# Kernel tuning notes

Hardware: AMD Instinct MI355X
Metric: run time of the kernel (lower is better)

Reference implementation:

```python
import jax, jax.numpy as jnp
import numpy as np
from jax.scipy.linalg import solve_triangular

B, L, HID, NH = 2, 1024, 1024, 4
DK = DV = 256
CONV_K, CHUNK, FIR_S_K, FIR_L_K = 4, 32, 3, 31
GATE_IN = HID + 3 * DV * 4 + DV * 4  # 5120
GATE_H = 2 * DV  # 512


def _l2norm(x):
    return x * jax.lax.rsqrt(jnp.sum(x * x, -1, keepdims=True) + 1e-6)


def _short_conv(x, w):
    # causal depthwise conv1d + silu. x: [b,l,c], w: [c,k]
    c, k = w.shape
    y = jax.lax.conv_general_dilated(x.transpose(0, 2, 1), w[:, None, :], (1,),
                                     [(k - 1, 0)], feature_group_count=c)
    return jax.nn.silu(y.transpose(0, 2, 1))


def _fir(x, f):
    # per-head depthwise causal FIR. x: [b,l,h,d], f: [h,d,k]
    b, l, h, d = x.shape
    k = f.shape[-1]
    xf = x.transpose(0, 2, 3, 1).reshape(b, h * d, l)
    y = jax.lax.conv_general_dilated(xf, f.reshape(h * d, 1, k), (1,),
                                     [(k - 1, 0)], feature_group_count=h * d)
    return y.reshape(b, h, d, l).transpose(0, 3, 1, 2)


def _delta_rule(q, k, v, beta, chunk=CHUNK):
    # q,k: [b,h,L,dk], v: [b,h,L,dv], beta: [b,h,L]; L % chunk == 0
    b, h, l, dk = q.shape
    dv = v.shape[-1]
    n = l // chunk
    q = _l2norm(q)
    k = _l2norm(k)
    v = v * beta[..., None]
    kb = k * beta[..., None]
    rs = lambda t: t.reshape(b, h, n, chunk, -1)
    q, k, v, kb = map(rs, (q, k, v, kb))
    # UT transform: serial forward substitution == unit-lower triangular solve
    A = -jnp.tril(jnp.einsum('bhncd,bhned->bhnce', kb, k), -1)  # strictly lower
    eye = jnp.eye(chunk, dtype=q.dtype)
    T = solve_triangular(eye - A, jnp.broadcast_to(eye, A.shape), lower=True)
    u = T @ v   # [b,h,n,c,dv]
    w = T @ kb  # [b,h,n,c,dk]
    mov = lambda t: jnp.moveaxis(t, 2, 0)

    def step(S, inp):
        qi, ki, ui, wi = inp  # [b,h,c,d]
        attn = jnp.tril(qi @ ki.transpose(0, 1, 3, 2))  # causal incl. diag
        u_i = ui - wi @ S
        o_i = qi @ S + attn @ u_i
        return S + ki.transpose(0, 1, 3, 2) @ u_i, o_i

    S0 = jnp.zeros((b, h, dk, dv), dtype=q.dtype)
    S, o = jax.lax.scan(step, S0, (mov(q), mov(k), mov(u), mov(w)))
    o = jnp.moveaxis(o, 0, 2).reshape(b, h, l, dv)
    return o, S


def _gate(hidden, branches, W1, b1, W2, b2, temp, eps_floor):
    def stats(p):
        m = p.mean(-1, keepdims=True)
        r = jnp.sqrt(jnp.clip((p * p).mean(-1, keepdims=True), 1e-8))
        mx = p.max(-1, keepdims=True)
        return jnp.concatenate([jnp.broadcast_to(m, p.shape),
                                jnp.broadcast_to(r, p.shape),
                                jnp.broadcast_to(mx, p.shape)], -1)

    b, l, h, d = branches[0].shape
    hb = jnp.broadcast_to(hidden[:, :, None, :], (b, l, h, hidden.shape[-1]))
    head_in = jnp.concatenate([hb] + [stats(p) for p in branches] + list(branches), -1)
    hmid = jax.nn.gelu(head_in @ W1 + b1, approximate=False)
    logits = hmid @ W2 + b2  # [b,l,h,4]
    t = jnp.clip(temp, 0.2, 10.0)[None, None, :, None]
    w = jax.nn.softmax(logits / t, -1)
    floor = jnp.clip(eps_floor, 1e-7, 0.1)[None, None]
    w = jnp.maximum(w, floor)
    return w / w.sum(-1, keepdims=True)


def setup_inputs() -> dict:
    key = jax.random.key(0)
    ks = jax.random.split(key, 16)
    s = 0.02
    inp = {
        'x': jax.random.normal(ks[0], (B, L, HID), jnp.float32),
        'Wq': jax.random.normal(ks[1], (HID, NH * DK), jnp.float32) * s,
        'Wk': jax.random.normal(ks[2], (HID, NH * DK), jnp.float32) * s,
        'Wv': jax.random.normal(ks[3], (HID, NH * DV), jnp.float32) * s,
        'Wb': jax.random.normal(ks[4], (HID, NH), jnp.float32) * s,
        'qc_w': jax.random.normal(ks[5], (NH * DK, CONV_K), jnp.float32) * 0.5,
        'kc_w': jax.random.normal(ks[6], (NH * DK, CONV_K), jnp.float32) * 0.5,
        'vc_w': jax.random.normal(ks[7], (NH * DV, CONV_K), jnp.float32) * 0.5,
        'gW1': jax.random.normal(ks[10], (GATE_IN, GATE_H), jnp.float32) * s,
        'gb1': jnp.zeros((GATE_H,), jnp.float32),
        'gW2': jax.random.normal(ks[11], (GATE_H, 4), jnp.float32) * s,
        'gb2': jnp.zeros((4,), jnp.float32),
        'temp': jnp.ones((NH,), jnp.float32),
        'eps_floor': jnp.full((NH, 4), 0.01, jnp.float32),
        'onorm_w': jnp.ones((DV,), jnp.float32),
        'Wo': jax.random.normal(ks[12], (NH * DV, HID), jnp.float32) * s,
    }
    # FIR filters: identity tap at last position + small noise (matches init intent)
    fs = jnp.zeros((NH, DV, FIR_S_K)).at[..., -1].set(1.0)
    fl = jnp.zeros((NH, DV, FIR_L_K)).at[..., -1].set(1.0)
    inp['fir_s'] = fs + s * jax.random.normal(ks[8], fs.shape, jnp.float32)
    inp['fir_l'] = fl + s * jax.random.normal(ks[9], fl.shape, jnp.float32)
    return inp


def reference(x, Wq, Wk, Wv, Wb, qc_w, kc_w, vc_w, fir_s, fir_l,
              gW1, gb1, gW2, gb2, temp, eps_floor, onorm_w, Wo):
    b, l, _ = x.shape
    q = _short_conv(x @ Wq, qc_w).reshape(b, l, NH, DK)
    k = _short_conv(x @ Wk, kc_w).reshape(b, l, NH, DK)
    v = _short_conv(x @ Wv, vc_w).reshape(b, l, NH, DV)
    beta = jax.nn.sigmoid(x @ Wb)  # [b,l,h]
    tr = lambda t: t.transpose(0, 2, 1, 3)
    delta_o, _ = _delta_rule(tr(q), tr(k), tr(v), beta.transpose(0, 2, 1))
    delta_o = tr(delta_o)  # [b,l,h,dv]
    branches = [_fir(v, fir_s), _fir(v, fir_l), delta_o, v]
    w = _gate(x, branches, gW1, gb1, gW2, gb2, temp, eps_floor)
    o = sum(w[..., i:i + 1] * branches[i] for i in range(4))
    o = o * jax.lax.rsqrt((o * o).mean(-1, keepdims=True) + 1e-5) * onorm_w
    return o.reshape(b, l, NH * DV) @ Wo
```

## Files before the change

kernel.cpp:

```cpp
#include <hip/hip_runtime.h>
#include <math.h>

#define BB 2
#define LL 1024
#define HIDD 1024
#define NH 4
#define DD 256
#define NCH 32
#define ROWS 2048
#define HROWS 8192

typedef long long i64;
typedef unsigned short u16t;
typedef unsigned int u32t;
typedef __attribute__((ext_vector_type(8))) short short8;
typedef __attribute__((ext_vector_type(4))) float f32x4;
#define MFMA_BF16(a, b, c) __builtin_amdgcn_mfma_f32_16x16x32_bf16(a, b, c, 0, 0, 0)

__device__ __forceinline__ float sigmoidf_(float x) { return 1.0f / (1.0f + expf(-x)); }

__device__ __forceinline__ u16t f2bf(float f) {
  u32t u = __float_as_uint(f);
  u = u + 0x7FFFu + ((u >> 16) & 1u);
  return (u16t)(u >> 16);
}
__device__ __forceinline__ u32t pk2(u16t a, u16t b) { return (u32t)a | ((u32t)b << 16); }

__device__ __forceinline__ u32t cvt_pk_bf16(float lo, float hi) {
  u32t r;
  asm("v_cvt_pk_bf16_f32 %0, %1, %2" : "=v"(r) : "v"(lo), "v"(hi));
  return r;
}

__device__ __forceinline__ void barrier_lds_only() {
  asm volatile("s_waitcnt lgkmcnt(0)" ::: "memory");
  __builtin_amdgcn_s_barrier();
  asm volatile("" ::: "memory");
}

template<int N>
__device__ __forceinline__ void block_reduce_sum(float* v, float* scratch) {
  int lane = threadIdx.x & 63, wid = threadIdx.x >> 6;
#pragma unroll
  for (int i = 0; i < N; i++) {
    float x = v[i];
#pragma unroll
    for (int off = 1; off < 64; off <<= 1) x += __shfl_xor(x, off);
    if (lane == 0) scratch[wid * N + i] = x;
  }
  __syncthreads();
#pragma unroll
  for (int i = 0; i < N; i++)
    v[i] = scratch[i] + scratch[N + i] + scratch[2 * N + i] + scratch[3 * N + i];
  __syncthreads();
}

__device__ __forceinline__ void transcast_body(
    const float* __restrict__ in, int ldin, u16t* __restrict__ out, int ldout,
    int nbi, int kbi, float (*tile)[33]) {
  int tx = threadIdx.x & 31, ty = threadIdx.x >> 5;
  int nb = nbi * 32, kb = kbi * 32;
#pragma unroll
  for (int r = 0; r < 4; r++)
    tile[ty + r * 8][tx] = in[(i64)(kb + ty + r * 8) * ldin + nb + tx];
  __syncthreads();
#pragma unroll
  for (int r = 0; r < 4; r++)
    out[(i64)(nb + ty + r * 8) * ldout + kb + tx] = f2bf(tile[tx][ty + r * 8]);
}

__global__ __launch_bounds__(256) void prep_kernel(
    const float* __restrict__ Wq, const float* __restrict__ Wk, const float* __restrict__ Wv,
    const float* __restrict__ x,
    u16t* __restrict__ WqkvT, u16t* __restrict__ xbf) {
  __shared__ float tile[32][33];
  int blk = blockIdx.x, t = threadIdx.x;
  if (blk < 3072) {
    int m = blk >> 10, bi = blk & 1023;
    const float* in = m == 0 ? Wq : m == 1 ? Wk : Wv;
    transcast_body(in, 1024, WqkvT + (i64)m * 1024 * 1024, 1024, bi & 31, bi >> 5, tile);
  } else {
    i64 e = ((i64)(blk - 3072) * 256 + t) * 4;
    float4 v = *(const float4*)(x + e);
    uint2 o;
    o.x = pk2(f2bf(v.x), f2bf(v.y));
    o.y = pk2(f2bf(v.z), f2bf(v.w));
    *(uint2*)(xbf + e) = o;
  }
}

__device__ __forceinline__ void gemm_bt_body(
    const u16t* __restrict__ A, const u16t* __restrict__ B,
    float* __restrict__ C, int K, int ldc, int n0, int m0,
    u16t* As, u16t* Bs) {
  int t = threadIdx.x;
  int w = t >> 6, lane = t & 63;
  int l15 = lane & 15, quad = lane >> 4;
  int wm = (w & 1) * 64, wn = (w >> 1) * 64;
  f32x4 acc[4][4] = {};
  int srow = t >> 1, shalf = (t & 1) * 16;
  const u16t* Ag = A + (i64)(m0 + srow) * K + shalf;
  const u16t* Bg = B + (i64)(n0 + srow) * K + shalf;
  for (int k0 = 0; k0 < K; k0 += 32) {
    *(uint4*)&As[srow * 40 + shalf] = *(const uint4*)(Ag + k0);
    *(uint4*)&As[srow * 40 + shalf + 8] = *(const uint4*)(Ag + k0 + 8);
    *(uint4*)&Bs[srow * 40 + shalf] = *(const uint4*)(Bg + k0);
    *(uint4*)&Bs[srow * 40 + shalf + 8] = *(const uint4*)(Bg + k0 + 8);
    __syncthreads();
    short8 a[4], b[4];
#pragma unroll
    for (int mt = 0; mt < 4; mt++)
      a[mt] = *(const short8*)&As[(wm + mt * 16 + l15) * 40 + quad * 8];
#pragma unroll
    for (int nt = 0; nt < 4; nt++)
      b[nt] = *(const short8*)&Bs[(wn + nt * 16 + l15) * 40 + quad * 8];
#pragma unroll
    for (int mt = 0; mt < 4; mt++)
#pragma unroll
      for (int nt = 0; nt < 4; nt++)
        acc[mt][nt] = MFMA_BF16(a[mt], b[nt], acc[mt][nt]);
    __syncthreads();
  }
#pragma unroll
  for (int mt = 0; mt < 4; mt++) {
    int r0 = m0 + wm + mt * 16 + quad * 4;
#pragma unroll
    for (int nt = 0; nt < 4; nt++) {
      int cc = n0 + wn + nt * 16 + l15;
#pragma unroll
      for (int rg = 0; rg < 4; rg++)
        C[(i64)(r0 + rg) * ldc + cc] = acc[mt][nt][rg];
    }
  }
}

__global__ __launch_bounds__(256) void gemm_bt_kernel(
    const u16t* __restrict__ A, const u16t* __restrict__ B,
    float* __restrict__ C, int K, int ldc) {
  __shared__ u16t As[128 * 40];
  __shared__ u16t Bs[128 * 40];
  gemm_bt_body(A, B, C, K, ldc, blockIdx.x * 128, blockIdx.y * 128, As, Bs);
}

__global__ __launch_bounds__(256) void conv_silu3_kernel(
    const float* __restrict__ pre, const float* __restrict__ qw,
    const float* __restrict__ kw, const float* __restrict__ vw,
    float* __restrict__ qo, float* __restrict__ ko, float* __restrict__ vo,
    u16t* __restrict__ brcat) {
  int seg = blockIdx.x >> 11;
  int row = blockIdx.x & 2047;
  int l = row & 1023;
  int c = threadIdx.x * 4;
  const float* w = seg == 0 ? qw : seg == 1 ? kw : vw;
  float* out = seg == 0 ? qo : seg == 1 ? ko : vo;
  float4 w0 = *(const float4*)(w + (i64)(c + 0) * 4);
  float4 w1 = *(const float4*)(w + (i64)(c + 1) * 4);
  float4 w2 = *(const float4*)(w + (i64)(c + 2) * 4);
  float4 w3 = *(const float4*)(w + (i64)(c + 3) * 4);
  const float* base = pre + (i64)row * 3072 + (seg << 10) + c;
  float4 x0 = *(const float4*)(base);
  float4 acc;
  acc.x = w0.w * x0.x; acc.y = w1.w * x0.y; acc.z = w2.w * x0.z; acc.w = w3.w * x0.w;
  if (l >= 1) {
    float4 xm = *(const float4*)(base - 3072);
    acc.x += w0.z * xm.x; acc.y += w1.z * xm.y; acc.z += w2.z * xm.z; acc.w += w3.z * xm.w;
  }
  if (l >= 2) {
    float4 xm = *(const float4*)(base - 2 * 3072);
    acc.x += w0.y * xm.x; acc.y += w1.y * xm.y; acc.z += w2.y * xm.z; acc.w += w3.y * xm.w;
  }
  if (l >= 3) {
    float4 xm = *(const float4*)(base - 3 * 3072);
    acc.x += w0.x * xm.x; acc.y += w1.x * xm.y; acc.z += w2.x * xm.z; acc.w += w3.x * xm.w;
  }
  float4 r;
  r.x = acc.x * sigmoidf_(acc.x);
  r.y = acc.y * sigmoidf_(acc.y);
  r.z = acc.z * sigmoidf_(acc.z);
  r.w = acc.w * sigmoidf_(acc.w);
  *(float4*)(out + (i64)row * 1024 + c) = r;
  if (seg == 2) {
    uint2 o;
    o.x = cvt_pk_bf16(r.x, r.y);
    o.y = cvt_pk_bf16(r.z, r.w);
    *(uint2*)(brcat + ((i64)row * 4 + (c >> 8)) * 1024 + 768 + (c & 255)) = o;
  }
}

__global__ __launch_bounds__(256) void beta_kernel(
    const float* __restrict__ x, const float* __restrict__ Wb, float* __restrict__ beta) {
  int row = blockIdx.x, t = threadIdx.x;
  __shared__ float sc[16];
  float a[4] = {0, 0, 0, 0};
  for (int c = t; c < 1024; c += 256) {
    float xv = x[(i64)row * 1024 + c];
    float4 wv = *(const float4*)(Wb + c * 4);
    a[0] += xv * wv.x; a[1] += xv * wv.y; a[2] += xv * wv.z; a[3] += xv * wv.w;
  }
  block_reduce_sum<4>(a, sc);
  if (t == 0) {
#pragma unroll
    for (int g = 0; g < 4; g++) beta[row * 4 + g] = sigmoidf_(a[g]);
  }
}

__global__ __launch_bounds__(256) void preprocess_kernel(
    const float* __restrict__ q, const float* __restrict__ k, const float* __restrict__ v,
    const float* __restrict__ beta, float* __restrict__ qn, float* __restrict__ kn,
    float* __restrict__ vb, float* __restrict__ kb, u16t* __restrict__ qnbf) {
  int t = threadIdx.x, lane = t & 63, wv = t >> 6;
  int row = blockIdx.x * 4 + wv;
  i64 base = (i64)row * 256 + lane * 4;
  float4 q4 = *(const float4*)(q + base);
  float4 k4 = *(const float4*)(k + base);
  float4 v4 = *(const float4*)(v + base);
  float s2[2];
  s2[0] = q4.x * q4.x + q4.y * q4.y + q4.z * q4.z + q4.w * q4.w;
  s2[1] = k4.x * k4.x + k4.y * k4.y + k4.z * k4.z + k4.w * k4.w;
#pragma unroll
  for (int off = 1; off < 64; off <<= 1) {
    s2[0] += __shfl_xor(s2[0], off);
    s2[1] += __shfl_xor(s2[1], off);
  }
  float qi = rsqrtf(s2[0] + 1e-6f), ki = rsqrtf(s2[1] + 1e-6f);
  float bet = beta[row];
  float4 qn4, kn4, vb4, kb4;
  qn4.x = q4.x * qi; qn4.y = q4.y * qi; qn4.z = q4.z * qi; qn4.w = q4.w * qi;
  kn4.x = k4.x * ki; kn4.y = k4.y * ki; kn4.z = k4.z * ki; kn4.w = k4.w * ki;
  vb4.x = v4.x * bet; vb4.y = v4.y * bet; vb4.z = v4.z * bet; vb4.w = v4.w * bet;
  kb4.x = kn4.x * bet; kb4.y = kn4.y * bet; kb4.z = kn4.z * bet; kb4.w = kn4.w * bet;
  *(float4*)(qn + base) = qn4;
  *(float4*)(kn + base) = kn4;
  *(float4*)(vb + base) = vb4;
  *(float4*)(kb + base) = kb4;
  int b = row >> 12, l = (row >> 2) & 1023, h = row & 3;
  uint2 o;
  o.x = cvt_pk_bf16(qn4.x, qn4.y);
  o.y = cvt_pk_bf16(qn4.z, qn4.w);
  *(uint2*)(qnbf + ((i64)(b * 4 + h) * 1024 + l) * 256 + lane * 4) = o;
}

__global__ __launch_bounds__(256) void phaseA_kernel(
    const float* __restrict__ qn, const float* __restrict__ kn,
    const float* __restrict__ vb, const float* __restrict__ kb,
    float* __restrict__ u_g, u16t* __restrict__ w_bf, u16t* __restrict__ attn_bf,
    u16t* __restrict__ knT) {
  __shared__ float KN[32][260];
  __shared__ float Ms[32][32];
  int blk = blockIdx.x, t = threadIdx.x;
  int i = blk & 31, bh = blk >> 5;
  int rbase = ((bh >> 2) * LL + i * 32) * NH + (bh & 3);
  i64 bhn = blk;
#pragma unroll
  for (int ii = 0; ii < 8; ii++) {
    int fid = t + ii * 256;
    int c = fid >> 6, dq = (fid & 63) << 2;
    *(float4*)&KN[c][dq] = *(const float4*)(kn + (i64)(rbase + c * NH) * 256 + dq);
  }
  __syncthreads();
  int c = t >> 3, e0 = (t & 7) * 4;
  const float* kbp = kb + (i64)(rbase + c * NH) * 256;
  const float* qp = qn + (i64)(rbase + c * NH) * 256;
  float am[4] = {0, 0, 0, 0}, aa[4] = {0, 0, 0, 0};
  for (int d = 0; d < 256; d += 4) {
    float4 kv = *(const float4*)(kbp + d);
    float4 qv = *(const float4*)(qp + d);
#pragma unroll
    for (int z = 0; z < 4; z++) {
      float4 nv = *(const float4*)&KN[e0 + z][d];
      am[z] += kv.x * nv.x + kv.y * nv.y + kv.z * nv.z + kv.w * nv.w;
      aa[z] += qv.x * nv.x + qv.y * nv.y + qv.z * nv.z + qv.w * nv.w;
    }
  }
  {
    uint2 o;
    u16t a0 = (e0 + 0 <= c) ? f2bf(aa[0]) : 0;
    u16t a1 = (e0 + 1 <= c) ? f2bf(aa[1]) : 0;
    u16t a2 = (e0 + 2 <= c) ? f2bf(aa[2]) : 0;
    u16t a3 = (e0 + 3 <= c) ? f2bf(aa[3]) : 0;
    o.x = pk2(a0, a1); o.y = pk2(a2, a3);
    *(uint2*)(attn_bf + bhn * 1024 + c * 32 + e0) = o;
  }
#pragma unroll
  for (int z = 0; z < 4; z++) {
    int e = e0 + z;
    Ms[c][e] = (e < c) ? am[z] : 0.0f;
  }
  __syncthreads();
  float uc[32], wc[32];
#pragma unroll
  for (int cc = 0; cc < 32; cc++) {
    float uval = vb[(i64)(rbase + cc * NH) * 256 + t];
    float wval = kb[(i64)(rbase + cc * NH) * 256 + t];
#pragma unroll
    for (int c2 = 0; c2 < cc; c2++) {
      float m = Ms[cc][c2];
      uval -= m * uc[c2];
      wval -= m * wc[c2];
    }
    uc[cc] = uval; wc[cc] = wval;
    u_g[(bhn * 32 + cc) * 256 + t] = uval;
    w_bf[(bhn * 32 + cc) * 256 + t] = f2bf(-wval);
  }
  int d = t;
  u16t o[32];
#pragma unroll
  for (int cc = 0; cc < 32; cc++) o[cc] = f2bf(KN[cc][d]);
#pragma unroll
  for (int z = 0; z < 4; z++) {
    uint4 vv;
    vv.x = pk2(o[z * 8 + 0], o[z * 8 + 1]);
    vv.y = pk2(o[z * 8 + 2], o[z * 8 + 3]);
    vv.z = pk2(o[z * 8 + 4], o[z * 8 + 5]);
    vv.w = pk2(o[z * 8 + 6], o[z * 8 + 7]);
    *(uint4*)(knT + (bhn * 256 + d) * 32 + z * 8) = vv;
  }
}

#define SROW 264
struct ScanBuf {
  short8 m8[8];
  f32x4 uc4;
  short8 af;
  short8 kf[4];
};

__device__ void delta_scan_body(
    int blk,
    const u16t* __restrict__ wbf, const u16t* __restrict__ knT,
    const float* __restrict__ u_g, const u16t* __restrict__ qnbf,
    const u16t* __restrict__ attnbf,
    float* __restrict__ dlt, u16t* __restrict__ brcat,
    u16t* Sbf, u16t* Ubf) {
  int t = threadIdx.x, w = t >> 6, lane = t & 63;
  int l15 = lane & 15, quad = lane >> 4;
  int bh = blk & 7, jb = blk >> 3, j0 = jb * 16;
  int b_ = bh >> 2, h_ = bh & 3;
  bool isU = (w < 2);
  int wc = isU ? w : (w - 2);
  for (int idx = t; idx < 16 * SROW; idx += 256) Sbf[idx] = 0;
  f32x4 accS[4] = {};
  __syncthreads();
  __builtin_amdgcn_s_setprio(1);

  auto load_chunk = [&](int i, ScanBuf& B) {
    i64 bhn = (i64)bh * 32 + i;
    const u16t* mbase = isU
        ? wbf + (bhn * 32 + wc * 16 + l15) * 256 + quad * 8
        : qnbf + ((i64)bh * 1024 + i * 32 + wc * 16 + l15) * 256 + quad * 8;
#pragma unroll
    for (int kd = 0; kd < 8; kd++) B.m8[kd] = *(const short8*)(mbase + kd * 32);
    if (isU) {
      int cm = wc * 16 + quad * 4;
#pragma unroll
      for (int r = 0; r < 4; r++)
        B.uc4[r] = u_g[(bhn * 32 + cm + r) * 256 + j0 + l15];
    } else {
      B.af = *(const short8*)(attnbf + bhn * 1024 + (wc * 16 + l15) * 32 + quad * 8);
    }
#pragma unroll
    for (int dt = 0; dt < 4; dt++)
      B.kf[dt] = *(const short8*)(knT + (bhn * 256 + w * 64 + dt * 16 + l15) * 32 + quad * 8);
  };

  auto process = [&](int i, ScanBuf& B) {
    f32x4 zero = {};
    f32x4 ca = isU ? B.uc4 : zero;
    f32x4 cb = zero;
#pragma unroll
    for (int kd = 0; kd < 4; kd++) {
      short8 sfa = *(const short8*)&Sbf[l15 * SROW + kd * 32 + quad * 8];
      short8 sfb = *(const short8*)&Sbf[l15 * SROW + (kd + 4) * 32 + quad * 8];
      ca = MFMA_BF16(B.m8[kd], sfa, ca);
      cb = MFMA_BF16(B.m8[kd + 4], sfb, cb);
    }
    f32x4 cacc;
#pragma unroll
    for (int r = 0; r < 4; r++) cacc[r] = ca[r] + cb[r];
    if (isU) {
      int cm = wc * 16 + quad * 4;
      uint2 o;
      o.x = cvt_pk_bf16(cacc[0], cacc[1]);
      o.y = cvt_pk_bf16(cacc[2], cacc[3]);
      *(uint2*)&Ubf[l15 * 40 + cm] = o;
    }
    barrier_lds_only();
    short8 bu = *(const short8*)&Ubf[l15 * 40 + quad * 8];
    if (!isU) {
      cacc = MFMA_BF16(B.af, bu, cacc);
#pragma unroll
      for (int rg = 0; rg < 4; rg++) {
        int l = i * 32 + wc * 16 + quad * 4 + rg;
        i64 row = ((i64)b_ * 1024 + l) * 4 + h_;
        dlt[row * 256 + j0 + l15] = cacc[rg];
        brcat[row * 1024 + 512 + j0 + l15] = f2bf(cacc[rg]);
      }
    }
#pragma unroll
    for (int dt = 0; dt < 4; dt++) accS[dt] = MFMA_BF16(B.kf[dt], bu, accS[dt]);
#pragma unroll
    for (int dt = 0; dt < 4; dt++) {
      uint2 o;
      o.x = cvt_pk_bf16(accS[dt][0], accS[dt][1]);
      o.y = cvt_pk_bf16(accS[dt][2], accS[dt][3]);
      *(uint2*)&Sbf[l15 * SROW + w * 64 + dt * 16 + quad * 4] = o;
    }
    barrier_lds_only();
  };

  ScanBuf b0, b1;
  load_chunk(0, b0);
#pragma unroll 1
  for (int ii = 0; ii < 16; ii++) {
    int i = ii * 2;
    load_chunk(i + 1, b1);
    process(i, b0);
    if (ii < 15) load_chunk(i + 2, b0);
    process(i + 1, b1);
  }
  __builtin_amdgcn_s_setprio(0);
}

__device__ void fir2_body(
    int blk, const float* __restrict__ v,
    const float* __restrict__ f_s, const float* __restrict__ f_l,
    float* __restrict__ fs, float* __restrict__ fl, u16t* __restrict__ brcat) {
  int t = threadIdx.x;
  int b = blk >> 8, h = (blk >> 6) & 3, lc = blk & 63;
  int l0 = lc * 16;
  float flw[31], fsw[3];
  const float* flp = f_l + ((i64)h * 256 + t) * 31;
#pragma unroll
  for (int j = 0; j < 31; j++) flw[j] = flp[j];
  const float* fsp = f_s + ((i64)h * 256 + t) * 3;
#pragma unroll
  for (int j = 0; j < 3; j++) fsw[j] = fsp[j];
  float win[46];
#pragma unroll
  for (int r = 0; r < 46; r++) {
    int l = l0 - 30 + r;
    win[r] = (l >= 0) ? v[(((i64)b * 1024 + l) * 4 + h) * 256 + t] : 0.0f;
  }
#pragma unroll
  for (int i = 0; i < 16; i++) {
    float al = 0.0f;
#pragma unroll
    for (int j = 0; j < 31; j++) al += flw[j] * win[i + j];
    float as = fsw[0] * win[i + 28] + fsw[1] * win[i + 29] + fsw[2] * win[i + 30];
    i64 row = ((i64)b * 1024 + (l0 + i)) * 4 + h;
    fs[row * 256 + t] = as;
    fl[row * 256 + t] = al;
    brcat[row * 1024 + t] = f2bf(as);
    brcat[row * 1024 + 256 + t] = f2bf(al);
  }
}

__global__ __launch_bounds__(256) void mega2_kernel(
    const u16t* __restrict__ wbf, const u16t* __restrict__ knT,
    const float* __restrict__ u_g, const u16t* __restrict__ qnbf,
    const u16t* __restrict__ attnbf, float* __restrict__ dlt, u16t* __restrict__ brcat,
    const float* __restrict__ vbuf, const float* __restrict__ firs,
    const float* __restrict__ firl, float* __restrict__ fs, float* __restrict__ fl,
    const float* __restrict__ gW1, const float* __restrict__ Wo,
    u16t* __restrict__ W1hT, u16t* __restrict__ W1bT, u16t* __restrict__ WoT,
    float* __restrict__ wsum) {
  __shared__ __attribute__((aligned(16))) char smem[9728];
  int blk = blockIdx.x;
  if (blk < 128) {
    u16t* Sbf = (u16t*)smem;
    u16t* Ubf = Sbf + 16 * SROW;
    delta_scan_body(blk, wbf, knT, u_g, qnbf, attnbf, dlt, brcat, Sbf, Ubf);
  } else if (blk < 640) {
    fir2_body(blk - 128, vbuf, firs, firl, fs, fl, brcat);
  } else if (blk < 2688) {
    float (*tile)[33] = (float(*)[33])smem;
    int pb = blk - 640;
    if (pb < 1024) {
      int which = pb >> 9, bi = pb & 511;
      const float* in = gW1 + (which ? (i64)4096 * 512 : 0);
      transcast_body(in, 512, which ? W1bT : W1hT, 1024, bi & 15, bi >> 4, tile);
    } else {
      int bi = pb - 1024;
      transcast_body(Wo, 1024, WoT, 1024, bi & 31, bi >> 5, tile);
    }
  } else {
    int bi = blk - 2688;
    int s12 = bi >> 1, col = (bi & 1) * 256 + threadIdx.x;
    const float* p = gW1 + (i64)(1024 + s12 * 256) * 512 + col;
    float acc = 0.0f;
    for (int r = 0; r < 256; r++) acc += p[(i64)r * 512];
    wsum[s12 * 512 + col] = acc;
  }
}

__global__ __launch_bounds__(256) void gemm2_kernel(
    const u16t* __restrict__ xbf, const u16t* __restrict__ W1hT,
    float* __restrict__ hbase,
    const u16t* __restrict__ brcat, const u16t* __restrict__ W1bT,
    float* __restrict__ branchW) {
  __shared__ u16t As[128 * 40];
  __shared__ u16t Bs[128 * 40];
  int blk = blockIdx.x;
  if (blk < 64) {
    gemm_bt_body(xbf, W1hT, hbase, 1024, 512, (blk & 3) * 128, (blk >> 2) * 128, As, Bs);
  } else {
    int bi = blk - 64;
    gemm_bt_body(brcat, W1bT, branchW, 1024, 512, (bi & 3) * 128, (bi >> 2) * 128, As, Bs);
  }
}

__global__ __launch_bounds__(256) void gatemix_kernel(
    const float* __restrict__ hbase, const float* __restrict__ brW,
    const float* __restrict__ wsum,
    const float* __restrict__ gb1, const float* __restrict__ gW2,
    const float* __restrict__ gb2, const float* __restrict__ temp,
    const float* __restrict__ epsf,
    const float* __restrict__ fs, const float* __restrict__ fl,
    const float* __restrict__ dlt, const float* __restrict__ v,
    const float* __restrict__ onw, u16t* __restrict__ out) {
  int t = threadIdx.x, lane = t & 63, wv = t >> 6;
  int row = blockIdx.x * 4 + wv;
  int bl = row >> 2, h = row & 3;
  i64 base = (i64)row * 256 + lane * 4;
  float4 vfs = *(const float4*)(fs + base);
  float4 vfl = *(const float4*)(fl + base);
  float4 vdl = *(const float4*)(dlt + base);
  float4 vvv = *(const float4*)(v + base);
  float r8[8];
  r8[0] = vfs.x + vfs.y + vfs.z + vfs.w;
  r8[1] = vfs.x * vfs.x + vfs.y * vfs.y + vfs.z * vfs.z + vfs.w * vfs.w;
  r8[2] = vfl.x + vfl.y + vfl.z + vfl.w;
  r8[3] = vfl.x * vfl.x + vfl.y * vfl.y + vfl.z * vfl.z + vfl.w * vfl.w;
  r8[4] = vdl.x + vdl.y + vdl.z + vdl.w;
  r8[5] = vdl.x * vdl.x + vdl.y * vdl.y + vdl.z * vdl.z + vdl.w * vdl.w;
  r8[6] = vvv.x + vvv.y + vvv.z + vvv.w;
  r8[7] = vvv.x * vvv.x + vvv.y * vvv.y + vvv.z * vvv.z + vvv.w * vvv.w;
#pragma unroll
  for (int off = 1; off < 64; off <<= 1) {
#pragma unroll
    for (int i = 0; i < 8; i++) r8[i] += __shfl_xor(r8[i], off);
  }
  float m4[4];
  m4[0] = fmaxf(fmaxf(vfs.x, vfs.y), fmaxf(vfs.z, vfs.w));
  m4[1] = fmaxf(fmaxf(vfl.x, vfl.y), fmaxf(vfl.z, vfl.w));
  m4[2] = fmaxf(fmaxf(vdl.x, vdl.y), fmaxf(vdl.z, vdl.w));
  m4[3] = fmaxf(fmaxf(vvv.x, vvv.y), fmaxf(vvv.z, vvv.w));
#pragma unroll
  for (int off = 1; off < 64; off <<= 1) {
#pragma unroll
    for (int i = 0; i < 4; i++) m4[i] = fmaxf(m4[i], __shfl_xor(m4[i], off));
  }
  float st[12];
#pragma unroll
  for (int p = 0; p < 4; p++) {
    st[p * 3 + 0] = r8[p * 2] * (1.0f / 256.0f);
    st[p * 3 + 1] = sqrtf(fmaxf(r8[p * 2 + 1] * (1.0f / 256.0f), 1e-8f));
    st[p * 3 + 2] = m4[p];
  }
  float lg[4] = {0, 0, 0, 0};
#pragma unroll
  for (int jj = 0; jj < 8; jj++) {
    int o = jj * 64 + lane;
    float hm = hbase[(i64)bl * 512 + o] + brW[(i64)row * 512 + o] + gb1[o];
#pragma unroll
    for (int s = 0; s < 12; s++) hm += st[s] * wsum[s * 512 + o];
    float ge = 0.5f * hm * (1.0f + erff(hm * 0.70710678118654752f));
    float4 w2 = *(const float4*)(gW2 + o * 4);
    lg[0] += ge * w2.x; lg[1] += ge * w2.y; lg[2] += ge * w2.z; lg[3] += ge * w2.w;
  }
#pragma unroll
  for (int off = 1; off < 64; off <<= 1) {
#pragma unroll
    for (int i = 0; i < 4; i++) lg[i] += __shfl_xor(lg[i], off);
  }
  float tt = fminf(fmaxf(temp[h], 0.2f), 10.0f);
  float l0 = (lg[0] + gb2[0]) / tt;
  float l1 = (lg[1] + gb2[1]) / tt;
  float l2 = (lg[2] + gb2[2]) / tt;
  float l3 = (lg[3] + gb2[3]) / tt;
  float m = fmaxf(fmaxf(l0, l1), fmaxf(l2, l3));
  float e0 = expf(l0 - m), e1 = expf(l1 - m), e2 = expf(l2 - m), e3 = expf(l3 - m);
  float ssum = e0 + e1 + e2 + e3;
  float w0 = e0 / ssum, w1 = e1 / ssum, w2 = e2 / ssum, w3 = e3 / ssum;
  w0 = fmaxf(w0, fminf(fmaxf(epsf[h * 4 + 0], 1e-7f), 0.1f));
  w1 = fmaxf(w1, fminf(fmaxf(epsf[h * 4 + 1], 1e-7f), 0.1f));
  w2 = fmaxf(w2, fminf(fmaxf(epsf[h * 4 + 2], 1e-7f), 0.1f));
  w3 = fmaxf(w3, fminf(fmaxf(epsf[h * 4 + 3], 1e-7f), 0.1f));
  float s2 = w0 + w1 + w2 + w3;
  float g0 = w0 / s2, g1 = w1 / s2, g2 = w2 / s2, g3 = w3 / s2;
  float4 o4;
  o4.x = g0 * vfs.x + g1 * vfl.x + g2 * vdl.x + g3 * vvv.x;
  o4.y = g0 * vfs.y + g1 * vfl.y + g2 * vdl.y + g3 * vvv.y;
  o4.z = g0 * vfs.z + g1 * vfl.z + g2 * vdl.z + g3 * vvv.z;
  o4.w = g0 * vfs.w + g1 * vfl.w + g2 * vdl.w + g3 * vvv.w;
  float ss = o4.x * o4.x + o4.y * o4.y + o4.z * o4.z + o4.w * o4.w;
#pragma unroll
  for (int off = 1; off < 64; off <<= 1) ss += __shfl_xor(ss, off);
  float scale = rsqrtf(ss * (1.0f / 256.0f) + 1e-5f);
  float4 ow4 = *(const float4*)(onw + lane * 4);
  uint2 ow;
  ow.x = cvt_pk_bf16(o4.x * scale * ow4.x, o4.y * scale * ow4.y);
  ow.y = cvt_pk_bf16(o4.z * scale * ow4.z, o4.w * scale * ow4.w);
  *(uint2*)(out + (i64)bl * 1024 + h * 256 + lane * 4) = ow;
}

extern "C" void kernel_launch(void* const* d_in, const int* in_sizes, int n_in,
                              void* d_out, int out_size, void* d_ws, size_t ws_size,
                              hipStream_t stream) {
  (void)in_sizes; (void)n_in; (void)out_size; (void)ws_size;
  const float* x    = (const float*)d_in[0];
  const float* Wq   = (const float*)d_in[1];
  const float* Wk   = (const float*)d_in[2];
  const float* Wv   = (const float*)d_in[3];
  const float* Wb   = (const float*)d_in[4];
  const float* qcw  = (const float*)d_in[5];
  const float* kcw  = (const float*)d_in[6];
  const float* vcw  = (const float*)d_in[7];
  const float* gW1  = (const float*)d_in[8];
  const float* gb1  = (const float*)d_in[9];
  const float* gW2  = (const float*)d_in[10];
  const float* gb2  = (const float*)d_in[11];
  const float* temp = (const float*)d_in[12];
  const float* epsf = (const float*)d_in[13];
  const float* onw  = (const float*)d_in[14];
  const float* Wo   = (const float*)d_in[15];
  const float* firs = (const float*)d_in[16];
  const float* firl = (const float*)d_in[17];
  float* out = (float*)d_out;

  float* ws = (float*)d_ws;
  float* qkv_pre  = ws + 0;
  float* branchW  = ws + 0;
  float* hbase    = ws + 4194304;
  u16t*  brcat    = (u16t*)(ws + 6291456);
  float* qbuf     = ws + 10485760; float* qn = qbuf;
  float* kbuf     = ws + 12582912; float* kn = kbuf;
  float* vbuf     = ws + 14680064;
  float* vb       = ws + 16777216;
  u16t*  omix_bf  = (u16t*)(ws + 16777216);
  u16t*  W1hT     = (u16t*)(ws + 17825792);
  u16t*  W1bT     = (u16t*)(ws + 18087936);
  u16t*  WoT      = (u16t*)(ws + 18350080);
  float* kb       = ws + 18874368;
  float* dlt      = ws + 18874368;
  float* u_g      = ws + 20971520;
  u16t*  w_bf     = (u16t*)(ws + 23068672);
  u16t*  qn_bf    = (u16t*)(ws + 24117248);
  u16t*  knT      = (u16t*)(ws + 25165824);
  u16t*  attn_bf  = (u16t*)(ws + 26214400);
  float* fs       = ws + 26345472;
  float* fl       = ws + 28442624;
  u16t*  xbf      = (u16t*)(ws + 30539776);
  u16t*  WqkvT    = (u16t*)(ws + 31588352);
  float* betab    = ws + 33161216;
  float* wsum     = ws + 33267712;

  prep_kernel<<<5120, 256, 0, stream>>>(Wq, Wk, Wv, x, WqkvT, xbf);
  gemm_bt_kernel<<<dim3(24, 16), 256, 0, stream>>>(xbf, WqkvT, qkv_pre, 1024, 3072);
  conv_silu3_kernel<<<6144, 256, 0, stream>>>(qkv_pre, qcw, kcw, vcw, qbuf, kbuf, vbuf, brcat);
  beta_kernel<<<2048, 256, 0, stream>>>(x, Wb, betab);
  preprocess_kernel<<<2048, 256, 0, stream>>>(qbuf, kbuf, vbuf, betab, qn, kn, vb, kb, qn_bf);
  phaseA_kernel<<<256, 256, 0, stream>>>(qn, kn, vb, kb, u_g, w_bf, attn_bf, knT);
  mega2_kernel<<<2712, 256, 0, stream>>>(w_bf, knT, u_g, qn_bf, attn_bf, dlt, brcat,
                                         vbuf, firs, firl, fs, fl,
                                         gW1, Wo, W1hT, W1bT, WoT, wsum);
  gemm2_kernel<<<320, 256, 0, stream>>>(xbf, W1hT, hbase, brcat, W1bT, branchW);
  gatemix_kernel<<<2048, 256, 0, stream>>>(hbase, branchW, wsum, gb1, gW2, gb2,
                                           temp, epsf, fs, fl, dlt, vbuf, onw, omix_bf);
  gemm_bt_kernel<<<dim3(8, 16), 256, 0, stream>>>(omix_bf, WoT, out, 1024, 1024);
}
```

Measured before the change: 342.1 us.

## Rebalance kernel fusion: fold beta into prep, overlap weight transposes and hidden GEMM

Merges the beta projection into the prep kernel, moves the gate/output weight transpose-casts and wsum reduction into the phaseA kernel (which only had 256 working blocks), and moves the hidden-state gate GEMM into the scan/FIR mega kernel. The branch GEMM becomes a standalone launch. The intent is to fill idle CUs during the low-parallelism phaseA and delta scan and to cut one launch, at the cost of larger shared memory in the merged kernels and workspace buffers relocated.

Result: no change. 342.8 us (+0.2%).

```diff
diff --git a/kernel.cpp b/kernel.cpp
--- a/kernel.cpp
+++ b/kernel.cpp
@@ -71,21 +71,34 @@
 
 __global__ __launch_bounds__(256) void prep_kernel(
     const float* __restrict__ Wq, const float* __restrict__ Wk, const float* __restrict__ Wv,
-    const float* __restrict__ x,
-    u16t* __restrict__ WqkvT, u16t* __restrict__ xbf) {
+    const float* __restrict__ x, const float* __restrict__ Wb,
+    u16t* __restrict__ WqkvT, u16t* __restrict__ xbf, float* __restrict__ betab) {
   __shared__ float tile[32][33];
   int blk = blockIdx.x, t = threadIdx.x;
   if (blk < 3072) {
     int m = blk >> 10, bi = blk & 1023;
     const float* in = m == 0 ? Wq : m == 1 ? Wk : Wv;
     transcast_body(in, 1024, WqkvT + (i64)m * 1024 * 1024, 1024, bi & 31, bi >> 5, tile);
-  } else {
+  } else if (blk < 5120) {
     i64 e = ((i64)(blk - 3072) * 256 + t) * 4;
     float4 v = *(const float4*)(x + e);
     uint2 o;
     o.x = pk2(f2bf(v.x), f2bf(v.y));
     o.y = pk2(f2bf(v.z), f2bf(v.w));
     *(uint2*)(xbf + e) = o;
+  } else {
+    int row = blk - 5120;
+    float a[4] = {0, 0, 0, 0};
+    for (int c = t; c < 1024; c += 256) {
+      float xv = x[(i64)row * 1024 + c];
+      float4 wv = *(const float4*)(Wb + c * 4);
+      a[0] += xv * wv.x; a[1] += xv * wv.y; a[2] += xv * wv.z; a[3] += xv * wv.w;
+    }
+    block_reduce_sum<4>(a, (float*)tile);
+    if (t == 0) {
+#pragma unroll
+      for (int g = 0; g < 4; g++) betab[row * 4 + g] = sigmoidf_(a[g]);
+    }
   }
 }
 
@@ -187,23 +200,6 @@
   }
 }
 
-__global__ __launch_bounds__(256) void beta_kernel(
-    const float* __restrict__ x, const float* __restrict__ Wb, float* __restrict__ beta) {
-  int row = blockIdx.x, t = threadIdx.x;
-  __shared__ float sc[16];
-  float a[4] = {0, 0, 0, 0};
-  for (int c = t; c < 1024; c += 256) {
-    float xv = x[(i64)row * 1024 + c];
-    float4 wv = *(const float4*)(Wb + c * 4);
-    a[0] += xv * wv.x; a[1] += xv * wv.y; a[2] += xv * wv.z; a[3] += xv * wv.w;
-  }
-  block_reduce_sum<4>(a, sc);
-  if (t == 0) {
-#pragma unroll
-    for (int g = 0; g < 4; g++) beta[row * 4 + g] = sigmoidf_(a[g]);
-  }
-}
-
 __global__ __launch_bounds__(256) void preprocess_kernel(
     const float* __restrict__ q, const float* __restrict__ k, const float* __restrict__ v,
     const float* __restrict__ beta, float* __restrict__ qn, float* __restrict__ kn,
@@ -240,80 +236,104 @@
   *(uint2*)(qnbf + ((i64)(b * 4 + h) * 1024 + l) * 256 + lane * 4) = o;
 }
 
-__global__ __launch_bounds__(256) void phaseA_kernel(
+__global__ __launch_bounds__(256) void phaseA2_kernel(
     const float* __restrict__ qn, const float* __restrict__ kn,
     const float* __restrict__ vb, const float* __restrict__ kb,
     float* __restrict__ u_g, u16t* __restrict__ w_bf, u16t* __restrict__ attn_bf,
-    u16t* __restrict__ knT) {
-  __shared__ float KN[32][260];
-  __shared__ float Ms[32][32];
+    u16t* __restrict__ knT,
+    const float* __restrict__ gW1, const float* __restrict__ Wo,
+    u16t* __restrict__ W1hT, u16t* __restrict__ W1bT, u16t* __restrict__ WoT,
+    float* __restrict__ wsum) {
+  __shared__ __attribute__((aligned(16))) char smem[37376];
   int blk = blockIdx.x, t = threadIdx.x;
-  int i = blk & 31, bh = blk >> 5;
-  int rbase = ((bh >> 2) * LL + i * 32) * NH + (bh & 3);
-  i64 bhn = blk;
-#pragma unroll
-  for (int ii = 0; ii < 8; ii++) {
-    int fid = t + ii * 256;
-    int c = fid >> 6, dq = (fid & 63) << 2;
-    *(float4*)&KN[c][dq] = *(const float4*)(kn + (i64)(rbase + c * NH) * 256 + dq);
-  }
-  __syncthreads();
-  int c = t >> 3, e0 = (t & 7) * 4;
-  const float* kbp = kb + (i64)(rbase + c * NH) * 256;
-  const float* qp = qn + (i64)(rbase + c * NH) * 256;
-  float am[4] = {0, 0, 0, 0}, aa[4] = {0, 0, 0, 0};
-  for (int d = 0; d < 256; d += 4) {
-    float4 kv = *(const float4*)(kbp + d);
-    float4 qv = *(const float4*)(qp + d);
+  if (blk < 256) {
+    float (*KN)[260] = (float(*)[260])smem;
+    float (*Ms)[32] = (float(*)[32])(smem + 33280);
+    int i = blk & 31, bh = blk >> 5;
+    int rbase = ((bh >> 2) * LL + i * 32) * NH + (bh & 3);
+    i64 bhn = blk;
+#pragma unroll
+    for (int ii = 0; ii < 8; ii++) {
+      int fid = t + ii * 256;
+      int c = fid >> 6, dq = (fid & 63) << 2;
+      *(float4*)&KN[c][dq] = *(const float4*)(kn + (i64)(rbase + c * NH) * 256 + dq);
+    }
+    __syncthreads();
+    int c = t >> 3, e0 = (t & 7) * 4;
+    const float* kbp = kb + (i64)(rbase + c * NH) * 256;
+    const float* qp = qn + (i64)(rbase + c * NH) * 256;
+    float am[4] = {0, 0, 0, 0}, aa[4] = {0, 0, 0, 0};
+    for (int d = 0; d < 256; d += 4) {
+      float4 kv = *(const float4*)(kbp + d);
+      float4 qv = *(const float4*)(qp + d);
+#pragma unroll
+      for (int z = 0; z < 4; z++) {
+        float4 nv = *(const float4*)&KN[e0 + z][d];
+        am[z] += kv.x * nv.x + kv.y * nv.y + kv.z * nv.z + kv.w * nv.w;
+        aa[z] += qv.x * nv.x + qv.y * nv.y + qv.z * nv.z + qv.w * nv.w;
+      }
+    }
+    {
+      uint2 o;
+      u16t a0 = (e0 + 0 <= c) ? f2bf(aa[0]) : 0;
+      u16t a1 = (e0 + 1 <= c) ? f2bf(aa[1]) : 0;
+      u16t a2 = (e0 + 2 <= c) ? f2bf(aa[2]) : 0;
+      u16t a3 = (e0 + 3 <= c) ? f2bf(aa[3]) : 0;
+      o.x = pk2(a0, a1); o.y = pk2(a2, a3);
+      *(uint2*)(attn_bf + bhn * 1024 + c * 32 + e0) = o;
+    }
 #pragma unroll
     for (int z = 0; z < 4; z++) {
-      float4 nv = *(const float4*)&KN[e0 + z][d];
-      am[z] += kv.x * nv.x + kv.y * nv.y + kv.z * nv.z + kv.w * nv.w;
-      aa[z] += qv.x * nv.x + qv.y * nv.y + qv.z * nv.z + qv.w * nv.w;
-    }
-  }
-  {
-    uint2 o;
-    u16t a0 = (e0 + 0 <= c) ? f2bf(aa[0]) : 0;
-    u16t a1 = (e0 + 1 <= c) ? f2bf(aa[1]) : 0;
-    u16t a2 = (e0 + 2 <= c) ? f2bf(aa[2]) : 0;
-    u16t a3 = (e0 + 3 <= c) ? f2bf(aa[3]) : 0;
-    o.x = pk2(a0, a1); o.y = pk2(a2, a3);
-    *(uint2*)(attn_bf + bhn * 1024 + c * 32 + e0) = o;
-  }
-#pragma unroll
-  for (int z = 0; z < 4; z++) {
-    int e = e0 + z;
-    Ms[c][e] = (e < c) ? am[z] : 0.0f;
-  }
-  __syncthreads();
-  float uc[32], wc[32];
-#pragma unroll
-  for (int cc = 0; cc < 32; cc++) {
-    float uval = vb[(i64)(rbase + cc * NH) * 256 + t];
-    float wval = kb[(i64)(rbase + cc * NH) * 256 + t];
-#pragma unroll
-    for (int c2 = 0; c2 < cc; c2++) {
-      float m = Ms[cc][c2];
-      uval -= m * uc[c2];
-      wval -= m * wc[c2];
-    }
-    uc[cc] = uval; wc[cc] = wval;
-    u_g[(bhn * 32 + cc) * 256 + t] = uval;
-    w_bf[(bhn * 32 + cc) * 256 + t] = f2bf(-wval);
-  }
-  int d = t;
-  u16t o[32];
-#pragma unroll
-  for (int cc = 0; cc < 32; cc++) o[cc] = f2bf(KN[cc][d]);
-#pragma unroll
-  for (int z = 0; z < 4; z++) {
-    uint4 vv;
-    vv.x = pk2(o[z * 8 + 0], o[z * 8 + 1]);
-    vv.y = pk2(o[z * 8 + 2], o[z * 8 + 3]);
-    vv.z = pk2(o[z * 8 + 4], o[z * 8 + 5]);
-    vv.w = pk2(o[z * 8 + 6], o[z * 8 + 7]);
-    *(uint4*)(knT + (bhn * 256 + d) * 32 + z * 8) = vv;
+      int e = e0 + z;
+      Ms[c][e] = (e < c) ? am[z] : 0.0f;
+    }
+    __syncthreads();
+    float uc[32], wc[32];
+#pragma unroll
+    for (int cc = 0; cc < 32; cc++) {
+      float uval = vb[(i64)(rbase + cc * NH) * 256 + t];
+      float wval = kb[(i64)(rbase + cc * NH) * 256 + t];
+#pragma unroll
+      for (int c2 = 0; c2 < cc; c2++) {
+        float m = Ms[cc][c2];
+        uval -= m * uc[c2];
+        wval -= m * wc[c2];
+      }
+      uc[cc] = uval; wc[cc] = wval;
+      u_g[(bhn * 32 + cc) * 256 + t] = uval;
+      w_bf[(bhn * 32 + cc) * 256 + t] = f2bf(-wval);
+    }
+    int d = t;
+    u16t o[32];
+#pragma unroll
+    for (int cc = 0; cc < 32; cc++) o[cc] = f2bf(KN[cc][d]);
+#pragma unroll
+    for (int z = 0; z < 4; z++) {
+      uint4 vv;
+      vv.x = pk2(o[z * 8 + 0], o[z * 8 + 1]);
+      vv.y = pk2(o[z * 8 + 2], o[z * 8 + 3]);
+      vv.z = pk2(o[z * 8 + 4], o[z * 8 + 5]);
+      vv.w = pk2(o[z * 8 + 6], o[z * 8 + 7]);
+      *(uint4*)(knT + (bhn * 256 + d) * 32 + z * 8) = vv;
+    }
+  } else if (blk < 2304) {
+    float (*tile)[33] = (float(*)[33])smem;
+    int pb = blk - 256;
+    if (pb < 1024) {
+      int which = pb >> 9, bi = pb & 511;
+      const float* in = gW1 + (which ? (i64)4096 * 512 : 0);
+      transcast_body(in, 512, which ? W1bT : W1hT, 1024, bi & 15, bi >> 4, tile);
+    } else {
+      int bi = pb - 1024;
+      transcast_body(Wo, 1024, WoT, 1024, bi & 31, bi >> 5, tile);
+    }
+  } else {
+    int bi = blk - 2304;
+    int s12 = bi >> 1, col = (bi & 1) * 256 + t;
+    const float* p = gW1 + (i64)(1024 + s12 * 256) * 512 + col;
+    float acc = 0.0f;
+    for (int r = 0; r < 256; r++) acc += p[(i64)r * 512];
+    wsum[s12 * 512 + col] = acc;
   }
 }
 
@@ -455,16 +475,15 @@
   }
 }
 
-__global__ __launch_bounds__(256) void mega2_kernel(
+__global__ __launch_bounds__(256) void mega5_kernel(
     const u16t* __restrict__ wbf, const u16t* __restrict__ knT,
     const float* __restrict__ u_g, const u16t* __restrict__ qnbf,
     const u16t* __restrict__ attnbf, float* __restrict__ dlt, u16t* __restrict__ brcat,
     const float* __restrict__ vbuf, const float* __restrict__ firs,
     const float* __restrict__ firl, float* __restrict__ fs, float* __restrict__ fl,
-    const float* __restrict__ gW1, const float* __restrict__ Wo,
-    u16t* __restrict__ W1hT, u16t* __restrict__ W1bT, u16t* __restrict__ WoT,
-    float* __restrict__ wsum) {
-  __shared__ __attribute__((aligned(16))) char smem[9728];
+    const u16t* __restrict__ xbf, const u16t* __restrict__ W1hT,
+    float* __restrict__ hbase) {
+  __shared__ __attribute__((aligned(16))) char smem[20480];
   int blk = blockIdx.x;
   if (blk < 128) {
     u16t* Sbf = (u16t*)smem;
@@ -472,40 +491,11 @@
     delta_scan_body(blk, wbf, knT, u_g, qnbf, attnbf, dlt, brcat, Sbf, Ubf);
   } else if (blk < 640) {
     fir2_body(blk - 128, vbuf, firs, firl, fs, fl, brcat);
-  } else if (blk < 2688) {
-    float (*tile)[33] = (float(*)[33])smem;
-    int pb = blk - 640;
-    if (pb < 1024) {
-      int which = pb >> 9, bi = pb & 511;
-      const float* in = gW1 + (which ? (i64)4096 * 512 : 0);
-      transcast_body(in, 512, which ? W1bT : W1hT, 1024, bi & 15, bi >> 4, tile);
-    } else {
-      int bi = pb - 1024;
-      transcast_body(Wo, 1024, WoT, 1024, bi & 31, bi >> 5, tile);
-    }
   } else {
-    int bi = blk - 2688;
-    int s12 = bi >> 1, col = (bi & 1) * 256 + threadIdx.x;
-    const float* p = gW1 + (i64)(1024 + s12 * 256) * 512 + col;
-    float acc = 0.0f;
-    for (int r = 0; r < 256; r++) acc += p[(i64)r * 512];
-    wsum[s12 * 512 + col] = acc;
-  }
-}
-
-__global__ __launch_bounds__(256) void gemm2_kernel(
-    const u16t* __restrict__ xbf, const u16t* __restrict__ W1hT,
-    float* __restrict__ hbase,
-    const u16t* __restrict__ brcat, const u16t* __restrict__ W1bT,
-    float* __restrict__ branchW) {
-  __shared__ u16t As[128 * 40];
-  __shared__ u16t Bs[128 * 40];
-  int blk = blockIdx.x;
-  if (blk < 64) {
-    gemm_bt_body(xbf, W1hT, hbase, 1024, 512, (blk & 3) * 128, (blk >> 2) * 128, As, Bs);
-  } else {
-    int bi = blk - 64;
-    gemm_bt_body(brcat, W1bT, branchW, 1024, 512, (bi & 3) * 128, (bi >> 2) * 128, As, Bs);
+    int bi = blk - 640;
+    u16t* As = (u16t*)smem;
+    u16t* Bs = As + 128 * 40;
+    gemm_bt_body(xbf, W1hT, hbase, 1024, 512, (bi & 3) * 128, (bi >> 2) * 128, As, Bs);
   }
 }
 
@@ -632,15 +622,15 @@
   float* qkv_pre  = ws + 0;
   float* branchW  = ws + 0;
   float* hbase    = ws + 4194304;
+  u16t*  W1hT     = (u16t*)(ws + 5242880);
+  u16t*  W1bT     = (u16t*)(ws + 5505024);
+  u16t*  WoT      = (u16t*)(ws + 5767168);
   u16t*  brcat    = (u16t*)(ws + 6291456);
   float* qbuf     = ws + 10485760; float* qn = qbuf;
   float* kbuf     = ws + 12582912; float* kn = kbuf;
   float* vbuf     = ws + 14680064;
   float* vb       = ws + 16777216;
   u16t*  omix_bf  = (u16t*)(ws + 16777216);
-  u16t*  W1hT     = (u16t*)(ws + 17825792);
-  u16t*  W1bT     = (u16t*)(ws + 18087936);
-  u16t*  WoT      = (u16t*)(ws + 18350080);
   float* kb       = ws + 18874368;
   float* dlt      = ws + 18874368;
   float* u_g      = ws + 20971520;
@@ -655,16 +645,16 @@
   float* betab    = ws + 33161216;
   float* wsum     = ws + 33267712;
 
-  prep_kernel<<<5120, 256, 0, stream>>>(Wq, Wk, Wv, x, WqkvT, xbf);
+  prep_kernel<<<7168, 256, 0, stream>>>(Wq, Wk, Wv, x, Wb, WqkvT, xbf, betab);
   gemm_bt_kernel<<<dim3(24, 16), 256, 0, stream>>>(xbf, WqkvT, qkv_pre, 1024, 3072);
   conv_silu3_kernel<<<6144, 256, 0, stream>>>(qkv_pre, qcw, kcw, vcw, qbuf, kbuf, vbuf, brcat);
-  beta_kernel<<<2048, 256, 0, stream>>>(x, Wb, betab);
   preprocess_kernel<<<2048, 256, 0, stream>>>(qbuf, kbuf, vbuf, betab, qn, kn, vb, kb, qn_bf);
-  phaseA_kernel<<<256, 256, 0, stream>>>(qn, kn, vb, kb, u_g, w_bf, attn_bf, knT);
-  mega2_kernel<<<2712, 256, 0, stream>>>(w_bf, knT, u_g, qn_bf, attn_bf, dlt, brcat,
-                                         vbuf, firs, firl, fs, fl,
-                                         gW1, Wo, W1hT, W1bT, WoT, wsum);
-  gemm2_kernel<<<320, 256, 0, stream>>>(xbf, W1hT, hbase, brcat, W1bT, branchW);
+  phaseA2_kernel<<<2328, 256, 0, stream>>>(qn, kn, vb, kb, u_g, w_bf, attn_bf, knT,
+                                           gW1, Wo, W1hT, W1bT, WoT, wsum);
+  mega5_kernel<<<704, 256, 0, stream>>>(w_bf, knT, u_g, qn_bf, attn_bf, dlt, brcat,
+                                        vbuf, firs, firl, fs, fl,
+                                        xbf, W1hT, hbase);
+  gemm_bt_kernel<<<dim3(4, 64), 256, 0, stream>>>(brcat, W1bT, branchW, 1024, 512);
   gatemix_kernel<<<2048, 256, 0, stream>>>(hbase, branchW, wsum, gb1, gW2, gb2,
                                            temp, epsf, fs, fl, dlt, vbuf, onw, omix_bf);
   gemm_bt_kernel<<<dim3(8, 16), 256, 0, stream>>>(omix_bf, WoT, out, 1024, 1024);
```
